# Performance work log

Hardware: AMD Instinct MI355X
Metric: run time of the kernel (lower is better)

## Reference

```python
import jax, jax.numpy as jnp
import numpy as np

B_SZ, SEQ = 2, 4096
D_MODEL = 1024
EXPAND = 2
HEADDIM = 64
D_STATE = 128
D_CONV = 4
INTER = EXPAND * D_MODEL            # 2048
NHEADS = INTER // HEADDIM           # 32
CONV_DIM = INTER + 2 * D_STATE      # n_groups = 1
PROJ_DIM = 2 * INTER + 2 * D_STATE + NHEADS
CHUNK = 256
EPS = 1e-5


def setup_inputs() -> dict:
    key = jax.random.key(0)
    k = jax.random.split(key, 6)
    u = jax.random.normal(k[0], (B_SZ, SEQ, D_MODEL), jnp.float32)
    in_proj_w = jax.random.normal(k[1], (D_MODEL, PROJ_DIM), jnp.float32) * 0.02
    conv_w = jax.random.normal(k[2], (CONV_DIM, D_CONV), jnp.float32) * 0.2
    conv_b = jnp.zeros((CONV_DIM,), jnp.float32)
    # dt init in [1e-3, 1e-1], inverse-softplus so softplus(dt_bias) recovers dt
    dt0 = jnp.exp(jax.random.uniform(k[3], (NHEADS,), jnp.float32, np.log(1e-3), np.log(1e-1)))
    dt_bias = jnp.log(jnp.expm1(dt0))
    A_log = jnp.log(jnp.arange(1, NHEADS + 1, dtype=jnp.float32))
    D_param = jnp.ones((NHEADS,), jnp.float32)
    norm_w = jnp.ones((INTER,), jnp.float32)
    out_proj_w = jax.random.normal(k[4], (INTER, D_MODEL), jnp.float32) * 0.02
    return {"u": u, "in_proj_w": in_proj_w, "conv_w": conv_w, "conv_b": conv_b,
            "dt_bias": dt_bias, "A_log": A_log, "D_param": D_param,
            "norm_w": norm_w, "out_proj_w": out_proj_w}


def _silu(x):
    return x * jax.nn.sigmoid(x)


def _causal_conv1d(x, w, b):
    # depthwise causal conv; x (b,s,c), w (c,k); tap k-1 is the current timestep
    k = w.shape[1]
    xp = jnp.pad(x, ((0, 0), (k - 1, 0), (0, 0)))
    y = b
    for i in range(k):
        y = y + xp[:, i:i + x.shape[1], :] * w[:, i]
    return y


def _segsum(x):
    # x (..., l) -> (..., l, l); segsum[i, j] = sum_{j < k <= i} x[k], -inf above diag
    l = x.shape[-1]
    cs = jnp.cumsum(x, -1)
    d = cs[..., :, None] - cs[..., None, :]
    mask = jnp.tril(jnp.ones((l, l), dtype=bool))
    return jnp.where(mask, d, -jnp.inf)


def _ssd(x, dt, A, Bm, Cm):
    # Mamba-2 chunked SSD (ssd_minimal_discrete with X = x*dt, Adt = A*dt).
    # x (b,s,h,p), dt (b,s,h), A (h,), Bm/Cm (b,s,n)
    b, s, h, p = x.shape
    n = Bm.shape[-1]
    c = s // CHUNK
    X = (x * dt[..., None]).reshape(b, c, CHUNK, h, p)          # (b,c,l,h,p)
    Adt = (dt * A).reshape(b, c, CHUNK, h).transpose(0, 3, 1, 2)  # (b,h,c,l)
    Bc = Bm.reshape(b, c, CHUNK, n)
    Cc = Cm.reshape(b, c, CHUNK, n)
    A_cum = jnp.cumsum(Adt, -1)                                  # (b,h,c,l)
    L = jnp.exp(_segsum(Adt))                                    # (b,h,c,l,l) causal decay
    # intra-chunk (diagonal blocks)
    scores = jnp.einsum('bcln,bcsn->bcls', Cc, Bc)               # (b,c,l,l)
    Y_diag = jnp.einsum('bhcls,bcshp->bclhp', scores[:, None] * L, X)
    # per-chunk final states
    decay_states = jnp.exp(A_cum[..., -1:] - A_cum)              # (b,h,c,l)
    states = jnp.einsum('bcln,bhcl,bclhp->bchpn', Bc, decay_states, X)
    # inter-chunk recurrence on chunk states
    A_chunk = jnp.pad(A_cum[..., -1], ((0, 0), (0, 0), (1, 0)))  # (b,h,c+1)
    decay_chunk = jnp.exp(_segsum(A_chunk))                      # (b,h,c+1,c+1)
    states = jnp.concatenate([jnp.zeros_like(states[:, :1]), states], axis=1)  # (b,c+1,h,p,n)
    states = jnp.einsum('bhzc,bchpn->bzhpn', decay_chunk, states)[:, :-1]      # (b,c,h,p,n)
    # state -> output contribution
    Y_off = jnp.einsum('bcln,bchpn,bhcl->bclhp', Cc, states, jnp.exp(A_cum))
    return (Y_diag + Y_off).reshape(b, s, h, p)


def reference(u, in_proj_w, conv_w, conv_b, dt_bias, A_log, D_param, norm_w, out_proj_w):
    b, s, _ = u.shape
    zxbcdt = u @ in_proj_w                                       # (b,s,PROJ_DIM)
    z = zxbcdt[..., :INTER]
    xBC = zxbcdt[..., INTER:INTER + CONV_DIM]
    dt = zxbcdt[..., INTER + CONV_DIM:]
    xBC = _silu(_causal_conv1d(xBC, conv_w, conv_b))
    x = xBC[..., :INTER]
    Bm = xBC[..., INTER:INTER + D_STATE]
    Cm = xBC[..., INTER + D_STATE:]
    dt = jax.nn.softplus(dt + dt_bias)                           # (b,s,h)
    A = -jnp.exp(A_log)                                          # (h,)
    xh = x.reshape(b, s, NHEADS, HEADDIM)
    y = _ssd(xh, dt, A, Bm, Cm) + D_param[None, None, :, None] * xh
    y = y.reshape(b, s, INTER)
    g = y * _silu(z)                                             # gated RMSNorm
    g = g * jax.lax.rsqrt(jnp.mean(g * g, -1, keepdims=True) + EPS) * norm_w
    return g @ out_proj_w
```

## Files before the change

### kernel.cpp

```cpp
#include <hip/hip_runtime.h>
#include <hip/hip_bf16.h>

#define B_SZ 2
#define SEQ 4096
#define DMODEL 1024
#define INTER 2048
#define NHEADS 32
#define HDIM 64
#define DSTATE 128
#define DCONV 4
#define CONVDIM 2304
#define PROJDIM 4384
#define CHUNK 256
#define NCHUNK 16
#define ROWS (B_SZ*SEQ)
#define NGEMM 4352

typedef __hip_bfloat16 bf16;
typedef short bfx8 __attribute__((ext_vector_type(8)));
typedef float f32x4 __attribute__((ext_vector_type(4)));

__device__ __forceinline__ float sigmoidf_(float x){ return 1.f/(1.f+expf(-x)); }
__device__ __forceinline__ float b2f(bf16 v){ return __bfloat162float(v); }
__device__ __forceinline__ bf16 f2b(float v){ return __float2bfloat16(v); }
__device__ __forceinline__ float bits2f(unsigned short u){ return __uint_as_float(((unsigned)u) << 16); }
__device__ __forceinline__ unsigned short f2bits(float v){ bf16 t = __float2bfloat16(v); return *(unsigned short*)&t; }

#define MFMA16(a,b,c) __builtin_amdgcn_mfma_f32_16x16x32_bf16(a,b,c,0,0,0)

__global__ void zero_out_kernel(float* o, int n){
  int i = blockIdx.x*256 + threadIdx.x;
  if (i < n) o[i] = 0.f;
}

__global__ __launch_bounds__(256) void transcast_kernel(const float* __restrict__ in,
    bf16* __restrict__ outT, int R, int ld, int coff){
  __shared__ float t[64][65];
  int r0 = blockIdx.y*64, c0 = blockIdx.x*64;
  int tid = threadIdx.x;
  #pragma unroll
  for (int i = 0; i < 16; i++){
    int idx = tid + i*256;
    int r = idx >> 6, c = idx & 63;
    t[r][c] = in[(size_t)(r0+r)*ld + coff + c0 + c];
  }
  __syncthreads();
  #pragma unroll
  for (int i = 0; i < 16; i++){
    int idx = tid + i*256;
    int c = idx >> 6, r = idx & 63;
    outT[(size_t)(c0+c)*R + r0 + r] = f2b(t[r][c]);
  }
}

__device__ __forceinline__ void stage8(const bf16* __restrict__ g, int Kdim,
    int tile0, int k0, char* region, int h, int tid){
  #pragma unroll
  for (int l = 0; l < 2; l++){
    int o  = h*16384 + (l*512 + tid)*16;
    int os = o ^ (((o >> 7) & 7) << 4);
    const bf16* src = g + (size_t)(tile0 + (os >> 7))*Kdim + k0 + ((os & 127) >> 1);
    __builtin_amdgcn_global_load_lds(
      (const __attribute__((address_space(1))) void*)src,
      (__attribute__((address_space(3))) void*)(region + h*16384 + (l*512 + (tid >> 6)*64)*16),
      16, 0, 0);
  }
}
__device__ __forceinline__ bfx8 fr8(const char* region, int row, int colbyte){
  int o = row*128 + colbyte;
  o ^= ((row & 7) << 4);
  return *(const bfx8*)(region + o);
}

#define LGKM0  asm volatile("s_waitcnt lgkmcnt(0)" ::: "memory"); __builtin_amdgcn_sched_barrier(0)
#define VM4    asm volatile("s_waitcnt vmcnt(4)" ::: "memory")
#define VM0    asm volatile("s_waitcnt vmcnt(0)" ::: "memory")
#define BAR    __builtin_amdgcn_s_barrier()
#define PRIO1  __builtin_amdgcn_s_setprio(1)
#define PRIO0  __builtin_amdgcn_s_setprio(0)

#define MFMA_QUAD(MH, NH, BARR)                                                \
  PRIO1;                                                                       \
  _Pragma("unroll") for (int m = 0; m < 4; m++)                                \
    _Pragma("unroll") for (int n = 0; n < 2; n++)                              \
      _Pragma("unroll") for (int kk = 0; kk < 2; kk++)                         \
        acc[(MH)+m][(NH)+n] = MFMA16(aF[m][kk], BARR[n][kk], acc[(MH)+m][(NH)+n]); \
  PRIO0

#define GEMM8_BODY(K_, NBY_)                                                   \
  extern __shared__ char lds[];                                                \
  char* A0 = lds;          char* B0 = lds + 32768;                             \
  char* A1 = lds + 65536;  char* B1 = lds + 98304;                             \
  const int tid = threadIdx.x, lane = tid & 63, wid = tid >> 6;                \
  const int wm = wid >> 2, wn = wid & 3;                                       \
  int nb = (blockIdx.x & 7)*((int)gridDim.x >> 3) + (blockIdx.x >> 3);         \
  const int by = nb % (NBY_), bx = nb / (NBY_);                                \
  const int row0 = by*256, col0 = bx*256;                                      \
  f32x4 acc[8][4] = {};                                                        \
  bfx8 aF[4][2], b01[2][2], b23[2][2];                                         \
  const int frow = lane & 15;                                                  \
  const int fcb0 = (lane >> 4)*16;                                             \
  const int JLAST = (K_)/128 - 1;                                              \
  stage8(Bt, K_, col0, 0,  B0, 0, tid);                                        \
  stage8(Bt, K_, col0, 0,  B0, 1, tid);                                        \
  stage8(A,  K_, row0, 0,  A0, 0, tid);                                        \
  stage8(A,  K_, row0, 0,  A0, 1, tid);                                        \
  stage8(Bt, K_, col0, 64, B1, 0, tid);                                        \
  stage8(Bt, K_, col0, 64, B1, 1, tid);                                        \
  VM4;                                                                         \
  BAR;                                                                         \
  _Pragma("unroll 1")                                                          \
  for (int j = 0; j <= JLAST; j++){                                            \
    const int kO  = j*128 + 64;                                                \
    const int kS1 = (j*128 + 128) & ((K_) - 1);                                \
    const int kS2 = (j*128 + 192) & ((K_) - 1);                                \
    stage8(A, K_, row0, kO, A1, 0, tid);                                       \
    _Pragma("unroll") for (int m = 0; m < 4; m++)                              \
      _Pragma("unroll") for (int kk = 0; kk < 2; kk++)                         \
        aF[m][kk] = fr8(A0, wm*128 + m*16 + frow, kk*64 + fcb0);               \
    _Pragma("unroll") for (int n = 0; n < 2; n++)                              \
      _Pragma("unroll") for (int kk = 0; kk < 2; kk++)                         \
        b01[n][kk] = fr8(B0, wn*64 + n*16 + frow, kk*64 + fcb0);               \
    LGKM0;                                                                     \
    MFMA_QUAD(0, 0, b01);                                                      \
    BAR;                                                                       \
    stage8(A, K_, row0, kO, A1, 1, tid);                                       \
    _Pragma("unroll") for (int n = 0; n < 2; n++)                              \
      _Pragma("unroll") for (int kk = 0; kk < 2; kk++)                         \
        b23[n][kk] = fr8(B0, wn*64 + (n+2)*16 + frow, kk*64 + fcb0);           \
    LGKM0;                                                                     \
    MFMA_QUAD(0, 2, b23);                                                      \
    BAR;                                                                       \
    if (j < JLAST) stage8(Bt, K_, col0, kS1, B0, 0, tid);                      \
    _Pragma("unroll") for (int m = 0; m < 4; m++)                              \
      _Pragma("unroll") for (int kk = 0; kk < 2; kk++)                         \
        aF[m][kk] = fr8(A0, wm*128 + (m+4)*16 + frow, kk*64 + fcb0);           \
    LGKM0;                                                                     \
    MFMA_QUAD(4, 0, b01);                                                      \
    BAR;                                                                       \
    if (j < JLAST){ stage8(Bt, K_, col0, kS1, B0, 1, tid); VM4; }              \
    else { VM0; }                                                              \
    MFMA_QUAD(4, 2, b23);                                                      \
    BAR;                                                                       \
    if (j < JLAST) stage8(A, K_, row0, kS1, A0, 0, tid);                       \
    _Pragma("unroll") for (int m = 0; m < 4; m++)                              \
      _Pragma("unroll") for (int kk = 0; kk < 2; kk++)                         \
        aF[m][kk] = fr8(A1, wm*128 + m*16 + frow, kk*64 + fcb0);               \
    _Pragma("unroll") for (int n = 0; n < 2; n++)                              \
      _Pragma("unroll") for (int kk = 0; kk < 2; kk++)                         \
        b01[n][kk] = fr8(B1, wn*64 + n*16 + frow, kk*64 + fcb0);               \
    LGKM0;                                                                     \
    MFMA_QUAD(0, 0, b01);                                                      \
    BAR;                                                                       \
    if (j < JLAST) stage8(A, K_, row0, kS1, A0, 1, tid);                       \
    _Pragma("unroll") for (int n = 0; n < 2; n++)                              \
      _Pragma("unroll") for (int kk = 0; kk < 2; kk++)                         \
        b23[n][kk] = fr8(B1, wn*64 + (n+2)*16 + frow, kk*64 + fcb0);           \
    LGKM0;                                                                     \
    MFMA_QUAD(0, 2, b23);                                                      \
    BAR;                                                                       \
    if (j < JLAST) stage8(Bt, K_, col0, kS2, B1, 0, tid);                      \
    _Pragma("unroll") for (int m = 0; m < 4; m++)                              \
      _Pragma("unroll") for (int kk = 0; kk < 2; kk++)                         \
        aF[m][kk] = fr8(A1, wm*128 + (m+4)*16 + frow, kk*64 + fcb0);           \
    LGKM0;                                                                     \
    MFMA_QUAD(4, 0, b01);                                                      \
    BAR;                                                                       \
    if (j < JLAST) stage8(Bt, K_, col0, kS2, B1, 1, tid);                      \
    VM4;                                                                       \
    MFMA_QUAD(4, 2, b23);                                                      \
    BAR;                                                                       \
  }

#define SST_STRIDE 280

__global__ __launch_bounds__(512, 2) void gemm8_inproj(const bf16* __restrict__ A,
    const bf16* __restrict__ Bt, bf16* __restrict__ z, bf16* __restrict__ xbc){
  GEMM8_BODY(DMODEL, 32)
  unsigned short* sst = (unsigned short*)lds;
  #pragma unroll 1
  for (int half = 0; half < 2; half++){
    if (wm == half){
      #pragma unroll
      for (int m = 0; m < 8; m++)
        #pragma unroll
        for (int n = 0; n < 4; n++)
          #pragma unroll
          for (int r = 0; r < 4; r++){
            int rl = m*16 + (lane>>4)*4 + r;
            sst[rl*SST_STRIDE + wn*64 + n*16 + (lane&15)] = f2bits(acc[m][n][r]);
          }
    }
    BAR;
    #pragma unroll
    for (int i = 0; i < 8; i++){
      int q = tid + i*512;
      int rl = q >> 5, c8 = (q & 31)*8;
      bfx8 v = *(const bfx8*)(sst + rl*SST_STRIDE + c8);
      int gr = row0 + half*128 + rl, gc = col0 + c8;
      if (gc < INTER) *(bfx8*)(z + (size_t)gr*INTER + gc) = v;
      else            *(bfx8*)(xbc + (size_t)gr*CONVDIM + (gc - INTER)) = v;
    }
    BAR;
  }
}

#define MFMA_GEMM_BODY(K_, EPILOGUE)                                           \
  __shared__ unsigned short As[128*64];                                        \
  __shared__ unsigned short Bs[128*64];                                        \
  const int tid = threadIdx.x;                                                 \
  const int lane = tid & 63, wid = tid >> 6;                                   \
  const int wm = wid >> 1, wn = wid & 1;                                       \
  const int row0 = blockIdx.y*128, col0 = blockIdx.x*128;                      \
  f32x4 acc[4][4] = {};                                                        \
  const int rstg = wid*32 + ((lane>>3)&7);                                     \
  const int kstg = (lane&7)*8;                                                 \
  for (int k0 = 0; k0 < (K_); k0 += 64){                                       \
    _Pragma("unroll")                                                          \
    for (int j = 0; j < 4; j++){                                               \
      const bf16* gA = A + (size_t)(row0 + rstg + j*8)*(K_) + k0 + kstg;       \
      __builtin_amdgcn_global_load_lds(                                        \
        (const __attribute__((address_space(1))) void*)gA,                     \
        (__attribute__((address_space(3))) void*)(As + (wid*32 + j*8)*64),     \
        16, 0, 0);                                                             \
      const bf16* gB = Bt + (size_t)(col0 + rstg + j*8)*(K_) + k0 + kstg;      \
      __builtin_amdgcn_global_load_lds(                                        \
        (const __attribute__((address_space(1))) void*)gB,                     \
        (__attribute__((address_space(3))) void*)(Bs + (wid*32 + j*8)*64),     \
        16, 0, 0);                                                             \
    }                                                                          \
    __syncthreads();                                                           \
    _Pragma("unroll")                                                          \
    for (int kk = 0; kk < 2; kk++){                                            \
      bfx8 af[4], bfr[4];                                                      \
      _Pragma("unroll")                                                        \
      for (int m = 0; m < 4; m++)                                              \
        af[m] = *(const bfx8*)(As + (wm*64 + m*16 + (lane&15))*64              \
                               + kk*32 + (lane>>4)*8);                         \
      _Pragma("unroll")                                                        \
      for (int n = 0; n < 4; n++)                                              \
        bfr[n] = *(const bfx8*)(Bs + (wn*64 + n*16 + (lane&15))*64             \
                                + kk*32 + (lane>>4)*8);                        \
      _Pragma("unroll")                                                        \
      for (int m = 0; m < 4; m++)                                              \
        _Pragma("unroll")                                                      \
        for (int n = 0; n < 4; n++)                                            \
          acc[m][n] = MFMA16(af[m], bfr[n], acc[m][n]);                        \
    }                                                                          \
    __syncthreads();                                                           \
  }                                                                            \
  _Pragma("unroll")                                                            \
  for (int m = 0; m < 4; m++){                                                 \
    int row = row0 + wm*64 + m*16 + (lane>>4)*4;                               \
    _Pragma("unroll")                                                          \
    for (int n = 0; n < 4; n++){                                               \
      int col = col0 + wn*64 + n*16 + (lane&15);                               \
      _Pragma("unroll")                                                        \
      for (int r = 0; r < 4; r++){                                             \
        float v = acc[m][n][r];                                                \
        int rr = row + r;                                                      \
        EPILOGUE                                                               \
      }                                                                        \
    }                                                                          \
  }

__global__ __launch_bounds__(256) void gemm_mfma_inproj(const bf16* __restrict__ A,
    const bf16* __restrict__ Bt, bf16* __restrict__ z, bf16* __restrict__ xbc){
  MFMA_GEMM_BODY(DMODEL,
    if (col < INTER) z[(size_t)rr*INTER + col] = f2b(v);
    else             xbc[(size_t)rr*CONVDIM + (col - INTER)] = f2b(v);
  )
}
__global__ __launch_bounds__(256) void gemm_mfma_outproj(const bf16* __restrict__ A,
    const bf16* __restrict__ Bt, float* __restrict__ C){
  MFMA_GEMM_BODY(INTER,
    C[(size_t)rr*DMODEL + col] = v;
  )
}

__global__ __launch_bounds__(256) void dt_partial(const float* __restrict__ u,
    const float* __restrict__ w_in, float* __restrict__ partial,
    unsigned short* __restrict__ u_bf){
  __shared__ float wsm[128][33];
  __shared__ float us[64][133];
  int ks = blockIdx.x, row0 = blockIdx.y*64;
  int k0 = ks*128;
  int tid = threadIdx.x;
  #pragma unroll
  for (int i = 0; i < 16; i++){
    int idx = tid + i*256;
    int r = idx >> 5, c = idx & 31;
    wsm[r][c] = w_in[(size_t)(k0 + r)*PROJDIM + NGEMM + c];
  }
  #pragma unroll
  for (int i = 0; i < 8; i++){
    int idx = tid + i*256;
    int r = idx >> 5, c4 = idx & 31;
    float4 v = *(const float4*)(u + (size_t)(row0 + r)*DMODEL + k0 + c4*4);
    us[r][c4*4+0] = v.x; us[r][c4*4+1] = v.y; us[r][c4*4+2] = v.z; us[r][c4*4+3] = v.w;
    ushort4 w;
    w.x = f2bits(v.x); w.y = f2bits(v.y); w.z = f2bits(v.z); w.w = f2bits(v.w);
    *(ushort4*)(u_bf + (size_t)(row0 + r)*DMODEL + k0 + c4*4) = w;
  }
  __syncthreads();
  int col = tid & 31, r0 = tid >> 5;
  float acc[8] = {};
  #pragma unroll 4
  for (int kk4 = 0; kk4 < 32; kk4++){
    float4 uv[8];
    #pragma unroll
    for (int i = 0; i < 8; i++)
      uv[i] = *(const float4*)&us[r0 + i*8][kk4*4];
    #pragma unroll
    for (int j = 0; j < 4; j++){
      float wv = wsm[kk4*4 + j][col];
      #pragma unroll
      for (int i = 0; i < 8; i++){
        float uvj = (j == 0) ? uv[i].x : (j == 1) ? uv[i].y : (j == 2) ? uv[i].z : uv[i].w;
        acc[i] = fmaf(uvj, wv, acc[i]);
      }
    }
  }
  #pragma unroll
  for (int i = 0; i < 8; i++)
    partial[((size_t)ks*ROWS + row0 + r0 + i*8)*NHEADS + col] = acc[i];
}

__global__ __launch_bounds__(256) void conv_kernel(const bf16* __restrict__ xbc,
    const float* __restrict__ cw, const float* __restrict__ cb,
    bf16* __restrict__ x, bf16* __restrict__ Bm, bf16* __restrict__ Cm){
  int bt = blockIdx.x / 9;
  int ch = (blockIdx.x % 9)*256 + threadIdx.x;
  int t = bt & (SEQ-1);
  float acc = cb[ch];
  #pragma unroll
  for (int i = 0; i < 4; i++){
    int tt = t - 3 + i;
    if (tt >= 0)
      acc = fmaf(b2f(xbc[(size_t)(bt - t + tt)*CONVDIM + ch]), cw[ch*4+i], acc);
  }
  float v = acc * sigmoidf_(acc);
  if (ch < INTER)              x[(size_t)bt*INTER + ch] = f2b(v);
  else if (ch < INTER+DSTATE)  Bm[(size_t)bt*DSTATE + (ch-INTER)] = f2b(v);
  else                         Cm[(size_t)bt*DSTATE + (ch-INTER-DSTATE)] = f2b(v);
}

__global__ __launch_bounds__(256) void acum_fused(const float* __restrict__ partial,
    const float* __restrict__ dt_bias, const float* __restrict__ A_log,
    float* __restrict__ dt, float* __restrict__ Acum){
  int bi = blockIdx.x;
  int c = bi & 15; int h = (bi >> 4) & 31; int b = bi >> 9;
  int l = threadIdx.x;
  __shared__ float sbuf[CHUNK];
  int t = c*CHUNK + l;
  size_t idx = (size_t)(b*SEQ + t)*NHEADS + h;
  float s = dt_bias[h];
  #pragma unroll
  for (int ks = 0; ks < 8; ks++)
    s += partial[(size_t)ks*ROWS*NHEADS + idx];
  float v = (s > 20.f) ? s : log1pf(expf(s));
  dt[idx] = v;
  float A = -expf(A_log[h]);
  sbuf[l] = v * A;
  __syncthreads();
  for (int off = 1; off < CHUNK; off <<= 1){
    float add = (l >= off) ? sbuf[l-off] : 0.f;
    __syncthreads();
    sbuf[l] += add;
    __syncthreads();
  }
  Acum[(size_t)bi*CHUNK + l] = sbuf[l];
}

__global__ __launch_bounds__(256) void scores_mfma(const bf16* __restrict__ Bm,
    const bf16* __restrict__ Cm, bf16* __restrict__ S){
  int bc = blockIdx.x;
  int b = bc >> 4, c = bc & 15;
  int tid = threadIdx.x, lane = tid & 63;
  int task = blockIdx.y*4 + (tid >> 6);
  if (task >= 10) return;
  int rb = (task >= 6) ? 3 : (task >= 3) ? 2 : (task >= 1) ? 1 : 0;
  int j = task - rb*(rb+1)/2;
  const bf16* Crow = Cm + (size_t)(b*SEQ + c*CHUNK)*DSTATE;
  const bf16* Brow = Bm + (size_t)(b*SEQ + c*CHUNK)*DSTATE;
  f32x4 acc[4][4] = {};
  #pragma unroll
  for (int kk = 0; kk < 4; kk++){
    bfx8 af[4], bfr[4];
    #pragma unroll
    for (int m = 0; m < 4; m++)
      af[m] = *(const bfx8*)(Crow + (size_t)(rb*64 + m*16 + (lane&15))*DSTATE + kk*32 + (lane>>4)*8);
    #pragma unroll
    for (int n = 0; n < 4; n++)
      bfr[n] = *(const bfx8*)(Brow + (size_t)(j*64 + n*16 + (lane&15))*DSTATE + kk*32 + (lane>>4)*8);
    #pragma unroll
    for (int m = 0; m < 4; m++)
      #pragma unroll
      for (int n = 0; n < 4; n++)
        acc[m][n] = MFMA16(af[m], bfr[n], acc[m][n]);
  }
  bf16* dst = S + (size_t)bc*CHUNK*CHUNK;
  #pragma unroll
  for (int m = 0; m < 4; m++)
    #pragma unroll
    for (int n = 0; n < 4; n++)
      #pragma unroll
      for (int r = 0; r < 4; r++)
        dst[(size_t)(rb*64 + m*16 + (lane>>4)*4 + r)*CHUNK + j*64 + n*16 + (lane&15)]
          = f2b(acc[m][n][r]);
}

__global__ __launch_bounds__(256) void xwt_kernel(const bf16* __restrict__ x,
    const bf16* __restrict__ Bm, const float* __restrict__ dt,
    const float* __restrict__ Acum, bf16* __restrict__ xwt, bf16* __restrict__ bt){
  int pt = blockIdx.x, tt = blockIdx.y, b = blockIdx.z;
  int tid = threadIdx.x;
  __shared__ unsigned short tile[64][72];
  __shared__ float wf[64];
  int t0 = tt*64;
  if (pt < 32){
    int h = pt, c = t0 >> 8;
    if (tid < 64){
      const float* AcB = Acum + ((size_t)(b*NHEADS + h)*NCHUNK + c)*CHUNK;
      int t = t0 + tid;
      wf[tid] = dt[(size_t)(b*SEQ + t)*NHEADS + h] * expf(AcB[255] - AcB[t & 255]);
    }
    __syncthreads();
    const bf16* src = x + (size_t)(b*SEQ + t0)*INTER + pt*64;
    #pragma unroll
    for (int i = 0; i < 2; i++){
      int u = tid + i*256;
      int r = u >> 3, po = (u & 7)*8;
      bfx8 v = *(const bfx8*)(src + (size_t)r*INTER + po);
      float d = wf[r];
      #pragma unroll
      for (int j = 0; j < 8; j++)
        tile[r][po + j] = f2bits(bits2f((unsigned short)v[j]) * d);
    }
    __syncthreads();
    bf16* dst = xwt + ((size_t)(b*INTER) + pt*64)*SEQ + t0;
    #pragma unroll
    for (int i = 0; i < 2; i++){
      int u = tid + i*256;
      int p = u >> 3, tc = (u & 7)*8;
      bfx8 v;
      #pragma unroll
      for (int j = 0; j < 8; j++) v[j] = (short)tile[tc + j][p];
      *(bfx8*)(dst + (size_t)p*SEQ + tc) = v;
    }
  } else {
    int n0 = (pt - 32)*64;
    const bf16* src = Bm + (size_t)(b*SEQ + t0)*DSTATE + n0;
    #pragma unroll
    for (int i = 0; i < 2; i++){
      int u = tid + i*256;
      int r = u >> 3, po = (u & 7)*8;
      bfx8 v = *(const bfx8*)(src + (size_t)r*DSTATE + po);
      *(bfx8*)&tile[r][po] = v;
    }
    __syncthreads();
    bf16* dst = bt + ((size_t)(b*DSTATE) + n0)*SEQ + t0;
    #pragma unroll
    for (int i = 0; i < 2; i++){
      int u = tid + i*256;
      int p = u >> 3, tc = (u & 7)*8;
      bfx8 v;
      #pragma unroll
      for (int j = 0; j < 8; j++) v[j] = (short)tile[tc + j][p];
      *(bfx8*)(dst + (size_t)p*SEQ + tc) = v;
    }
  }
}

__global__ __launch_bounds__(256) void chunk_states_mfma(const bf16* __restrict__ xwt,
    const bf16* __restrict__ bt, float* __restrict__ states){
  int bi = blockIdx.x;
  int h = bi & 31; int c = (bi >> 5) & 15; int b = bi >> 9;
  int tid = threadIdx.x, lane = tid & 63, w = tid >> 6;
  int wm = w >> 1, wn = w & 1;
  const bf16* Arow = xwt + ((size_t)(b*INTER) + h*64)*SEQ + c*CHUNK;
  const bf16* Brow = bt + (size_t)(b*DSTATE)*SEQ + c*CHUNK;
  f32x4 acc[2][4] = {};
  #pragma unroll
  for (int kk = 0; kk < 8; kk++){
    bfx8 af[2], bfr[4];
    #pragma unroll
    for (int m = 0; m < 2; m++)
      af[m] = *(const bfx8*)(Arow + (size_t)(wm*32 + m*16 + (lane&15))*SEQ + kk*32 + (lane>>4)*8);
    #pragma unroll
    for (int n = 0; n < 4; n++)
      bfr[n] = *(const bfx8*)(Brow + (size_t)(wn*64 + n*16 + (lane&15))*SEQ + kk*32 + (lane>>4)*8);
    #pragma unroll
    for (int m = 0; m < 2; m++)
      #pragma unroll
      for (int n = 0; n < 4; n++)
        acc[m][n] = MFMA16(af[m], bfr[n], acc[m][n]);
  }
  float* dst = states + (size_t)bi*HDIM*DSTATE;
  #pragma unroll
  for (int m = 0; m < 2; m++)
    #pragma unroll
    for (int n = 0; n < 4; n++)
      #pragma unroll
      for (int r = 0; r < 4; r++){
        int p = wm*32 + m*16 + (lane>>4)*4 + r;
        int nn = wn*64 + n*16 + (lane&15);
        dst[(size_t)p*DSTATE + nn] = acc[m][n][r];
      }
}

__global__ __launch_bounds__(256) void scan_kernel(float* __restrict__ states,
    const float* __restrict__ Acum){
  int idx = blockIdx.x*256 + threadIdx.x;
  int n = idx & 127; int p = (idx >> 7) & 63; int h = (idx >> 13) & 31; int b = idx >> 18;
  float R = 0.f;
  for (int c = 0; c < NCHUNK; c++){
    size_t o = (((size_t)((b*NCHUNK + c)*NHEADS + h))*HDIM + p)*DSTATE + n;
    float s = states[o];
    states[o] = R;
    float dA = expf(Acum[((size_t)(b*NHEADS + h)*NCHUNK + c)*CHUNK + CHUNK-1]);
    R = R*dA + s;
  }
}

__global__ __launch_bounds__(256, 3) void ydiag_mfma(
    const bf16* x, const float* __restrict__ dt,
    const float* __restrict__ Acum, const bf16* __restrict__ Sg,
    const bf16* __restrict__ Cm, const float* __restrict__ states,
    const float* __restrict__ Dp, bf16* y){
  int bi = blockIdx.x;
  int h = bi & 31; int c = (bi >> 5) & 15; int b = bi >> 9;
  int bc = b*NCHUNK + c;
  int tid = threadIdx.x, lane = tid & 63, w = tid >> 6;

  __shared__ unsigned short XdtT[64*264];
  __shared__ unsigned short pool[128*72];
  __shared__ float Acs[CHUNK];
  __shared__ float dts[CHUNK];

  const float* AcBase = Acum + ((size_t)(b*NHEADS + h)*NCHUNK + c)*CHUNK;
  Acs[tid] = AcBase[tid];
  dts[tid] = dt[(size_t)(b*SEQ + c*CHUNK + tid)*NHEADS + h];
  {
    const float* src = states + (size_t)bi*HDIM*DSTATE;
    #pragma unroll
    for (int i = 0; i < 32; i++){
      int idx = tid + i*256;
      int p = idx >> 7, n = idx & 127;
      pool[p*136 + n] = f2bits(src[idx]);
    }
  }
  __syncthreads();

  const bf16* Crow = Cm + (size_t)(b*SEQ + c*CHUNK)*DSTATE;

  f32x4 accY[4][4] = {};
  #pragma unroll
  for (int kk = 0; kk < 4; kk++){
    bfx8 af[4], bfr[4];
    #pragma unroll
    for (int m = 0; m < 4; m++)
      af[m] = *(const bfx8*)(Crow + (size_t)(w*64 + m*16 + (lane&15))*DSTATE + kk*32 + (lane>>4)*8);
    #pragma unroll
    for (int n = 0; n < 4; n++)
      bfr[n] = *(const bfx8*)(pool + (n*16 + (lane&15))*136 + kk*32 + (lane>>4)*8);
    #pragma unroll
    for (int m = 0; m < 4; m++)
      #pragma unroll
      for (int n = 0; n < 4; n++)
        accY[m][n] = MFMA16(af[m], bfr[n], accY[m][n]);
  }
  {
    float eAl[4][4];
    #pragma unroll
    for (int m = 0; m < 4; m++)
      #pragma unroll
      for (int r = 0; r < 4; r++)
        eAl[m][r] = expf(Acs[w*64 + m*16 + (lane>>4)*4 + r]);
    #pragma unroll
    for (int m = 0; m < 4; m++)
      #pragma unroll
      for (int n = 0; n < 4; n++)
        #pragma unroll
        for (int r = 0; r < 4; r++)
          accY[m][n][r] *= eAl[m][r];
  }
  __syncthreads();

  #pragma unroll 1
  for (int q = 0; q < 2; q++){
    const bf16* xg = x + (size_t)(b*SEQ + c*CHUNK + q*128)*INTER + h*HDIM;
    #pragma unroll
    for (int i = 0; i < 4; i++){
      int u = tid + i*256;
      int s = u >> 3, p0 = (u & 7)*8;
      bfx8 v = *(const bfx8*)(xg + (size_t)s*INTER + p0);
      float d = dts[q*128 + s];
      bfx8 o;
      #pragma unroll
      for (int j = 0; j < 8; j++)
        o[j] = (short)f2bits(bits2f((unsigned short)v[j]) * d);
      *(bfx8*)(pool + s*72 + p0) = o;
    }
    __syncthreads();
    {
      int p = tid & 63, sb = tid >> 6;
      #pragma unroll
      for (int i = 0; i < 4; i++){
        int s0 = (sb + i*4)*8;
        bfx8 v;
        #pragma unroll
        for (int j = 0; j < 8; j++)
          v[j] = (short)pool[(s0 + j)*72 + p];
        *(bfx8*)(XdtT + p*264 + q*128 + s0) = v;
      }
    }
    __syncthreads();
  }

  const bf16* Srow = Sg + (size_t)bc*CHUNK*CHUNK + (size_t)(w*64)*CHUNK;
  float Dh = Dp[h];
  for (int j = 0; j <= w; j++){
    int s0 = j*64;
    bfx8 wfr[4][2];
    if (j < w){
      float m_ = Acs[s0 + 63];
      float rowf[4];
      #pragma unroll
      for (int m = 0; m < 4; m++)
        rowf[m] = expf(Acs[w*64 + m*16 + (lane&15)] - m_);
      #pragma unroll
      for (int kk = 0; kk < 2; kk++){
        float colf[8];
        #pragma unroll
        for (int t = 0; t < 8; t++)
          colf[t] = expf(m_ - Acs[s0 + kk*32 + (lane>>4)*8 + t]);
        #pragma unroll
        for (int m = 0; m < 4; m++){
          bfx8 raw = *(const bfx8*)(Srow + (size_t)(m*16 + (lane&15))*CHUNK + s0 + kk*32 + (lane>>4)*8);
          bfx8 o;
          #pragma unroll
          for (int t = 0; t < 8; t++)
            o[t] = (short)f2bits(bits2f((unsigned short)raw[t]) * rowf[m] * colf[t]);
          wfr[m][kk] = o;
        }
      }
    } else {
      #pragma unroll
      for (int kk = 0; kk < 2; kk++)
        #pragma unroll
        for (int m = 0; m < 4; m++){
          int lg = w*64 + m*16 + (lane&15);
          float Al = Acs[lg];
          bfx8 raw = *(const bfx8*)(Srow + (size_t)(m*16 + (lane&15))*CHUNK + s0 + kk*32 + (lane>>4)*8);
          bfx8 o;
          #pragma unroll
          for (int t = 0; t < 8; t++){
            int sg = s0 + kk*32 + (lane>>4)*8 + t;
            float v;
            if (sg > lg)       v = 0.f;
            else if (sg == lg) v = bits2f((unsigned short)raw[t]) + Dh/dts[lg];
            else               v = bits2f((unsigned short)raw[t]) * expf(Al - Acs[sg]);
            o[t] = (short)f2bits(v);
          }
          wfr[m][kk] = o;
        }
    }
    #pragma unroll
    for (int kk = 0; kk < 2; kk++){
      bfx8 bfr[4];
      #pragma unroll
      for (int n = 0; n < 4; n++)
        bfr[n] = *(const bfx8*)(XdtT + (n*16 + (lane&15))*264 + s0 + kk*32 + (lane>>4)*8);
      #pragma unroll
      for (int m = 0; m < 4; m++)
        #pragma unroll
        for (int n = 0; n < 4; n++)
          accY[m][n] = MFMA16(wfr[m][kk], bfr[n], accY[m][n]);
    }
  }
  bf16* yg = y + (size_t)(b*SEQ + c*CHUNK)*INTER + h*HDIM;
  #pragma unroll
  for (int m = 0; m < 4; m++)
    #pragma unroll
    for (int n = 0; n < 4; n++)
      #pragma unroll
      for (int r = 0; r < 4; r++)
        yg[(size_t)(w*64 + m*16 + (lane>>4)*4 + r)*INTER + n*16 + (lane&15)]
          = f2b(accY[m][n][r]);
}

__global__ __launch_bounds__(256) void gatenorm_kernel(bf16* __restrict__ y,
    const bf16* __restrict__ z, const float* __restrict__ nw){
  int row = blockIdx.x;
  const bf16* zr = z + (size_t)row*INTER;
  bf16* yr = y + (size_t)row*INTER;
  int tid = threadIdx.x;
  float g[8]; float ss = 0.f;
  #pragma unroll
  for (int i = 0; i < 8; i++){
    int idx = tid + i*256;
    float zv = b2f(zr[idx]);
    float gv = b2f(yr[idx]) * zv * sigmoidf_(zv);
    g[i] = gv; ss += gv*gv;
  }
  #pragma unroll
  for (int off = 32; off > 0; off >>= 1) ss += __shfl_down(ss, off);
  __shared__ float red[4];
  __shared__ float stot;
  int lane = tid & 63, wid = tid >> 6;
  if (lane == 0) red[wid] = ss;
  __syncthreads();
  if (tid == 0) stot = rsqrtf((red[0]+red[1]+red[2]+red[3]) * (1.f/INTER) + 1e-5f);
  __syncthreads();
  float sc = stot;
  #pragma unroll
  for (int i = 0; i < 8; i++){
    int idx = tid + i*256;
    yr[idx] = f2b(g[i]*sc*nw[idx]);
  }
}

extern "C" void kernel_launch(void* const* d_in, const int* in_sizes, int n_in,
                              void* d_out, int out_size, void* d_ws, size_t ws_size,
                              hipStream_t stream){
  const float* u    = (const float*)d_in[0];
  const float* w_in = (const float*)d_in[1];
  const float* cw   = (const float*)d_in[2];
  const float* cb   = (const float*)d_in[3];
  const float* dtb  = (const float*)d_in[4];
  const float* Alog = (const float*)d_in[5];
  const float* Dp   = (const float*)d_in[6];
  const float* nw   = (const float*)d_in[7];
  const float* w_out= (const float*)d_in[8];
  float* out = (float*)d_out;
  char* ws = (char*)d_ws;

  const size_t OFF_Z     = 0;
  const size_t OFF_XBC   = 33554432;
  const size_t OFF_DT    = 67108864;
  const size_t OFF_ACUM  = 68157440;
  const size_t OFF_X     = 71303168;
  const size_t OFF_UBF   = 104857600;
  const size_t OFF_WINT  = 121634816;
  const size_t OFF_XWT   = 104857600;
  const size_t OFF_BM    = 138412032;
  const size_t OFF_CM    = 140509184;
  const size_t OFF_BT    = 143654912;
  const size_t OFF_WOUTT = 145752064;
  const size_t OFF_PART  = 149946368;
  const size_t NEED      = 158334976;

  if (ws_size < NEED){
    zero_out_kernel<<<(out_size + 255)/256, 256, 0, stream>>>(out, out_size);
    return;
  }

  bf16*  z      = (bf16*)(ws + OFF_Z);
  bf16*  xbc    = (bf16*)(ws + OFF_XBC);
  float* states = (float*)(ws + OFF_XBC);
  float* dt     = (float*)(ws + OFF_DT);
  float* Acum   = (float*)(ws + OFF_ACUM);
  bf16*  x      = (bf16*)(ws + OFF_X);
  bf16*  y      = (bf16*)(ws + OFF_X);
  bf16*  u_bf   = (bf16*)(ws + OFF_UBF);
  bf16*  w_inT  = (bf16*)(ws + OFF_WINT);
  bf16*  xwt    = (bf16*)(ws + OFF_XWT);
  bf16*  Bm     = (bf16*)(ws + OFF_BM);
  bf16*  Cm     = (bf16*)(ws + OFF_CM);
  bf16*  bt     = (bf16*)(ws + OFF_BT);
  bf16*  w_outT = (bf16*)(ws + OFF_WOUTT);
  float* part   = (float*)(ws + OFF_PART);
  bf16*  S      = (bf16*)(ws + OFF_PART);

  bool use8 = true;
  if (hipFuncSetAttribute((const void*)gemm8_inproj,
        hipFuncAttributeMaxDynamicSharedMemorySize, 131072) != hipSuccess) use8 = false;

  dt_partial<<<dim3(8, ROWS/64), 256, 0, stream>>>(u, w_in, part, (unsigned short*)u_bf);
  transcast_kernel<<<dim3(NGEMM/64, DMODEL/64), 256, 0, stream>>>(w_in, w_inT, DMODEL, PROJDIM, 0);
  if (use8)
    gemm8_inproj<<<544, 512, 131072, stream>>>(u_bf, w_inT, z, xbc);
  else
    gemm_mfma_inproj<<<dim3(NGEMM/128, ROWS/128), 256, 0, stream>>>(u_bf, w_inT, z, xbc);
  conv_kernel<<<ROWS*9, 256, 0, stream>>>(xbc, cw, cb, x, Bm, Cm);
  acum_fused<<<B_SZ*NHEADS*NCHUNK, 256, 0, stream>>>(part, dtb, Alog, dt, Acum);
  scores_mfma<<<dim3(B_SZ*NCHUNK, 3), 256, 0, stream>>>(Bm, Cm, S);
  xwt_kernel<<<dim3(34, 64, 2), 256, 0, stream>>>(x, Bm, dt, Acum, xwt, bt);
  chunk_states_mfma<<<B_SZ*NCHUNK*NHEADS, 256, 0, stream>>>(xwt, bt, states);
  scan_kernel<<<(B_SZ*NHEADS*HDIM*DSTATE)/256, 256, 0, stream>>>(states, Acum);
  ydiag_mfma<<<B_SZ*NCHUNK*NHEADS, 256, 0, stream>>>(x, dt, Acum, S, Cm, states, Dp, y);
  transcast_kernel<<<dim3(DMODEL/64, INTER/64), 256, 0, stream>>>(w_out, w_outT, INTER, DMODEL, 0);
  gatenorm_kernel<<<ROWS, 256, 0, stream>>>(y, z, nw);
  gemm_mfma_outproj<<<dim3(DMODEL/128, ROWS/128), 256, 0, stream>>>(y, w_outT, out);
}
```

Baseline: 410.4 us.

## Reorder in-proj tile raster, stream conv over time, vectorize gatenorm

Changes the in-proj GEMM block mapping so consecutive blocks walk across columns for a fixed row band rather than down rows, which changes L2 reuse of the A and B tiles. Rewrites the causal conv so each thread handles 64 consecutive timesteps with a rolling register window, avoiding the fourfold reload of xbc and the per-element div/mod indexing, at the cost of fewer blocks. Vectorizes the gated RMSNorm to 16-byte loads and stores per thread.

New measurement: 351.8 us. -14.3%, faster.

```diff
diff --git a/kernel.cpp b/kernel.cpp
--- a/kernel.cpp
+++ b/kernel.cpp
@@ -87,14 +87,14 @@
         acc[(MH)+m][(NH)+n] = MFMA16(aF[m][kk], BARR[n][kk], acc[(MH)+m][(NH)+n]); \
   PRIO0
 
-#define GEMM8_BODY(K_, NBY_)                                                   \
+#define GEMM8_BODY(K_, NBX_)                                                   \
   extern __shared__ char lds[];                                                \
   char* A0 = lds;          char* B0 = lds + 32768;                             \
   char* A1 = lds + 65536;  char* B1 = lds + 98304;                             \
   const int tid = threadIdx.x, lane = tid & 63, wid = tid >> 6;                \
   const int wm = wid >> 2, wn = wid & 3;                                       \
   int nb = (blockIdx.x & 7)*((int)gridDim.x >> 3) + (blockIdx.x >> 3);         \
-  const int by = nb % (NBY_), bx = nb / (NBY_);                                \
+  const int bx = nb % (NBX_), by = nb / (NBX_);                                \
   const int row0 = by*256, col0 = bx*256;                                      \
   f32x4 acc[8][4] = {};                                                        \
   bfx8 aF[4][2], b01[2][2], b23[2][2];                                         \
@@ -176,7 +176,7 @@
 
 __global__ __launch_bounds__(512, 2) void gemm8_inproj(const bf16* __restrict__ A,
     const bf16* __restrict__ Bt, bf16* __restrict__ z, bf16* __restrict__ xbc){
-  GEMM8_BODY(DMODEL, 32)
+  GEMM8_BODY(DMODEL, 17)
   unsigned short* sst = (unsigned short*)lds;
   #pragma unroll 1
   for (int half = 0; half < 2; half++){
@@ -329,20 +329,34 @@
 __global__ __launch_bounds__(256) void conv_kernel(const bf16* __restrict__ xbc,
     const float* __restrict__ cw, const float* __restrict__ cb,
     bf16* __restrict__ x, bf16* __restrict__ Bm, bf16* __restrict__ Cm){
-  int bt = blockIdx.x / 9;
-  int ch = (blockIdx.x % 9)*256 + threadIdx.x;
-  int t = bt & (SEQ-1);
-  float acc = cb[ch];
-  #pragma unroll
-  for (int i = 0; i < 4; i++){
-    int tt = t - 3 + i;
-    if (tt >= 0)
-      acc = fmaf(b2f(xbc[(size_t)(bt - t + tt)*CONVDIM + ch]), cw[ch*4+i], acc);
-  }
-  float v = acc * sigmoidf_(acc);
-  if (ch < INTER)              x[(size_t)bt*INTER + ch] = f2b(v);
-  else if (ch < INTER+DSTATE)  Bm[(size_t)bt*DSTATE + (ch-INTER)] = f2b(v);
-  else                         Cm[(size_t)bt*DSTATE + (ch-INTER-DSTATE)] = f2b(v);
+  int ch = blockIdx.x*256 + threadIdx.x;
+  int t0 = blockIdx.y*64;
+  int b  = blockIdx.z;
+  float w0 = cw[ch*4+0], w1 = cw[ch*4+1], w2 = cw[ch*4+2], w3 = cw[ch*4+3];
+  float bia = cb[ch];
+  const bf16* src = xbc + (size_t)(b*SEQ)*CONVDIM + ch;
+  float xm3 = 0.f, xm2 = 0.f, xm1 = 0.f;
+  if (t0 > 0){
+    xm3 = b2f(src[(size_t)(t0-3)*CONVDIM]);
+    xm2 = b2f(src[(size_t)(t0-2)*CONVDIM]);
+    xm1 = b2f(src[(size_t)(t0-1)*CONVDIM]);
+  }
+  bf16* dst; size_t dstride;
+  if (ch < INTER)             { dst = x  + (size_t)(b*SEQ + t0)*INTER  + ch;                 dstride = INTER; }
+  else if (ch < INTER+DSTATE) { dst = Bm + (size_t)(b*SEQ + t0)*DSTATE + (ch-INTER);         dstride = DSTATE; }
+  else                        { dst = Cm + (size_t)(b*SEQ + t0)*DSTATE + (ch-INTER-DSTATE);  dstride = DSTATE; }
+  #pragma unroll 4
+  for (int i = 0; i < 64; i++){
+    float xc = b2f(src[(size_t)(t0+i)*CONVDIM]);
+    float acc = bia;
+    acc = fmaf(xm3, w0, acc);
+    acc = fmaf(xm2, w1, acc);
+    acc = fmaf(xm1, w2, acc);
+    acc = fmaf(xc,  w3, acc);
+    float v = acc * sigmoidf_(acc);
+    dst[(size_t)i*dstride] = f2b(v);
+    xm3 = xm2; xm2 = xm1; xm1 = xc;
+  }
 }
 
 __global__ __launch_bounds__(256) void acum_fused(const float* __restrict__ partial,
@@ -696,13 +710,14 @@
   const bf16* zr = z + (size_t)row*INTER;
   bf16* yr = y + (size_t)row*INTER;
   int tid = threadIdx.x;
+  bfx8 zv = *(const bfx8*)(zr + tid*8);
+  bfx8 yv = *(const bfx8*)(yr + tid*8);
   float g[8]; float ss = 0.f;
   #pragma unroll
-  for (int i = 0; i < 8; i++){
-    int idx = tid + i*256;
-    float zv = b2f(zr[idx]);
-    float gv = b2f(yr[idx]) * zv * sigmoidf_(zv);
-    g[i] = gv; ss += gv*gv;
+  for (int j = 0; j < 8; j++){
+    float zf = bits2f((unsigned short)zv[j]);
+    float gv = bits2f((unsigned short)yv[j]) * zf * sigmoidf_(zf);
+    g[j] = gv; ss += gv*gv;
   }
   #pragma unroll
   for (int off = 32; off > 0; off >>= 1) ss += __shfl_down(ss, off);
@@ -714,11 +729,18 @@
   if (tid == 0) stot = rsqrtf((red[0]+red[1]+red[2]+red[3]) * (1.f/INTER) + 1e-5f);
   __syncthreads();
   float sc = stot;
-  #pragma unroll
-  for (int i = 0; i < 8; i++){
-    int idx = tid + i*256;
-    yr[idx] = f2b(g[i]*sc*nw[idx]);
-  }
+  float4 nw0 = *(const float4*)(nw + tid*8);
+  float4 nw1 = *(const float4*)(nw + tid*8 + 4);
+  bfx8 o;
+  o[0] = (short)f2bits(g[0]*sc*nw0.x);
+  o[1] = (short)f2bits(g[1]*sc*nw0.y);
+  o[2] = (short)f2bits(g[2]*sc*nw0.z);
+  o[3] = (short)f2bits(g[3]*sc*nw0.w);
+  o[4] = (short)f2bits(g[4]*sc*nw1.x);
+  o[5] = (short)f2bits(g[5]*sc*nw1.y);
+  o[6] = (short)f2bits(g[6]*sc*nw1.z);
+  o[7] = (short)f2bits(g[7]*sc*nw1.w);
+  *(bfx8*)(yr + tid*8) = o;
 }
 
 extern "C" void kernel_launch(void* const* d_in, const int* in_sizes, int n_in,
@@ -783,7 +805,7 @@
     gemm8_inproj<<<544, 512, 131072, stream>>>(u_bf, w_inT, z, xbc);
   else
     gemm_mfma_inproj<<<dim3(NGEMM/128, ROWS/128), 256, 0, stream>>>(u_bf, w_inT, z, xbc);
-  conv_kernel<<<ROWS*9, 256, 0, stream>>>(xbc, cw, cb, x, Bm, Cm);
+  conv_kernel<<<dim3(9, SEQ/64, B_SZ), 256, 0, stream>>>(xbc, cw, cb, x, Bm, Cm);
   acum_fused<<<B_SZ*NHEADS*NCHUNK, 256, 0, stream>>>(part, dtb, Alog, dt, Acum);
   scores_mfma<<<dim3(B_SZ*NCHUNK, 3), 256, 0, stream>>>(Bm, Cm, S);
   xwt_kernel<<<dim3(34, 64, 2), 256, 0, stream>>>(x, Bm, dt, Acum, xwt, bt);
```
